# Kernel optimization log

Measured on AMD Instinct MI355X. Metric: run time of the kernel, lower is better.

The kernel has to match this reference:

```python
import jax, jax.numpy as jnp
import numpy as np

H, W = 56, 56
N = H * W
C = 2
THETA_ALPHA = 160.0
THETA_BETA = 3.0
THETA_GAMMA = 3.0
NUM_ITERATIONS = 10


def setup_inputs() -> dict:
    key = jax.random.key(0)
    k1, k2, k3, k4 = jax.random.split(key, 4)
    inputs = jax.random.uniform(k1, (2, H, W), dtype=jnp.float32)
    # Keras 'uniform' initializer: U(-0.05, 0.05)
    sp_w = jax.random.uniform(k2, (C, C), minval=-0.05, maxval=0.05, dtype=jnp.float32)
    bl_w = jax.random.uniform(k3, (C, C), minval=-0.05, maxval=0.05, dtype=jnp.float32)
    compat = jax.random.uniform(k4, (C, C), minval=-0.05, maxval=0.05, dtype=jnp.float32)
    return {"inputs": inputs, "spatial_ker_weights": sp_w,
            "bilateral_ker_weights": bl_w, "compatibility_matrix": compat}


def _sqdist(f):
    # f: [N, D] -> [N, N] squared pairwise distances
    s = jnp.sum(f * f, axis=1)
    return s[:, None] + s[None, :] - 2.0 * (f @ f.T)


def _kernels(rgb_flat):
    # rgb_flat: [N, 3] pixel colors (0..255)
    ys, xs = jnp.meshgrid(jnp.arange(H, dtype=jnp.float32),
                          jnp.arange(W, dtype=jnp.float32), indexing="ij")
    pos = jnp.stack([xs.reshape(-1), ys.reshape(-1)], axis=1)  # [N, 2]
    # spatial (Gaussian) kernel: exp(-||p-q||^2 / (2*gamma^2))
    k_sp = jnp.exp(-0.5 * _sqdist(pos / THETA_GAMMA))
    # bilateral kernel: positions scaled by alpha, colors by beta
    f_bl = jnp.concatenate([pos / THETA_ALPHA, rgb_flat / THETA_BETA], axis=1)
    k_bl = jnp.exp(-0.5 * _sqdist(f_bl))
    return k_sp, k_bl


def reference(inputs, spatial_ker_weights, bilateral_ker_weights, compatibility_matrix):
    unary = inputs[0]            # [H, W], foreground prob
    gray = inputs[1] * 255.0     # [H, W], image intensities scaled as in the layer

    # unaries: [C, H, W] with channel 0 = 1-u, channel 1 = u
    unaries = jnp.stack([1.0 - unary, unary], axis=0).reshape(C, N)

    rgb_flat = jnp.tile(gray.reshape(-1)[:, None], (1, 3))  # [N, 3]

    k_sp, k_bl = _kernels(rgb_flat)
    ones = jnp.ones((N,), dtype=jnp.float32)
    norm_sp = k_sp @ ones  # [N]
    norm_bl = k_bl @ ones  # [N]

    q = unaries
    for i in range(NUM_ITERATIONS):
        softmax_out = q if i == 0 else jax.nn.softmax(q, axis=0)
        spatial_out = (softmax_out @ k_sp) / norm_sp[None, :]     # [C, N]
        bilateral_out = (softmax_out @ k_bl) / norm_bl[None, :]   # [C, N]
        message = spatial_ker_weights @ spatial_out + bilateral_ker_weights @ bilateral_out
        pairwise = compatibility_matrix @ message                 # [C, N]
        q = unaries - pairwise

    cur_q = q.reshape(C, H, W).transpose(1, 2, 0)  # [H, W, C]
    obj_prob = jax.nn.softmax(cur_q, axis=2)[:, :, 1]
    return obj_prob.reshape(1, H, W)
```

## Files before the change

kernel.cpp:

```cpp
#include <hip/hip_runtime.h>


namespace {

constexpr int NPIX = 3136;
constexpr int WIMG = 56;
constexpr int JPB  = 16;
constexpr int NBLK = NPIX / JPB;
constexpr int NTHR = 512;
constexpr int NQ   = NPIX / 4;
constexpr int NBUF = 9;
constexpr int BAND = 16;
constexpr int Q2   = NQ - NTHR;

constexpr float LOG2E = 1.4426950408889634f;
constexpr float C1 = -LOG2E / 18.0f;
constexpr float C2 = -LOG2E / 51200.0f;
constexpr float C3 = -LOG2E / 6.0f;

constexpr int O_SSH  = 0;
constexpr int O_GSRT = 12544;
constexpr int O_MSRT = 25088;
constexpr int O_OFF  = 31360;
constexpr int O_WSX  = 32400;
constexpr int O_WSY  = 35984;
constexpr int O_ROWC = 39568;
constexpr int POOLSZ = 43376;

#define REDUCE32(v) \
    { v += __shfl_xor(v, 1); v += __shfl_xor(v, 2); v += __shfl_xor(v, 4); \
      v += __shfl_xor(v, 8); v += __shfl_xor(v, 16); }

__global__ __launch_bounds__(NTHR) void crf_all(
    const float* __restrict__ inp,
    const float* __restrict__ spw, const float* __restrict__ blw,
    const float* __restrict__ cmw,
    float* sbufs, float* __restrict__ out)
{
    __shared__ __align__(16) unsigned char pool[POOLSZ];
    float*  s_sh  = (float*)(pool + O_SSH);
    float4* s_sh4 = (float4*)(pool + O_SSH);
    float*  g_srt = (float*)(pool + O_GSRT);
    unsigned short* m_srt = (unsigned short*)(pool + O_MSRT);
    unsigned*       offs  = (unsigned*)(pool + O_OFF);
    float*  wsx   = (float*)(pool + O_WSX);
    float*  wsy   = (float*)(pool + O_WSY);
    float*  rowc  = (float*)(pool + O_ROWC);
    unsigned short* H  = (unsigned short*)(pool + O_SSH);
    unsigned*       Hz = (unsigned*)(pool + O_SSH);

    const int t   = threadIdx.x;
    const int bid = blockIdx.x;
    const int sub = t & 31;
    const int jl  = t >> 5;
    const int j   = bid * JPB + jl;
    const int xj  = j % WIMG;
    const int yj  = j / WIMG;
    const float xjf = (float)xj, yjf = (float)yj;

    const float uj = inp[j];
    const float gj = inp[NPIX + j] * 255.0f;

    const float e0 = cmw[2] - cmw[0];
    const float e1 = cmw[3] - cmw[1];
    const float alpha = e0 * (spw[0] + blw[0]) + e1 * (spw[2] + blw[2]);
    const float beta  = e0 * (spw[1] - spw[0]) + e1 * (spw[3] - spw[2]);
    const float gamma = e0 * (blw[1] - blw[0]) + e1 * (blw[3] - blw[2]);

    for (int i = t; i < 6272; i += NTHR) Hz[i] = 0u;
    for (int idx = t; idx < JPB * 56; idx += NTHR) {
        const int jlw = idx / 56, p = idx - jlw * 56;
        const int jj = bid * JPB + jlw;
        const float ddx = (float)(jj % WIMG - p);
        const float ddy = (float)(jj / WIMG - p);
        wsx[idx] = __builtin_amdgcn_exp2f(C1 * ddx * ddx);
        wsy[idx] = __builtin_amdgcn_exp2f(C1 * ddy * ddy);
    }
    __syncthreads();
    if (t < 49) {
        unsigned short* Hr = H + t * 256;
        const int mb = t * 64;
        for (int i = 0; i < 64; ++i) {
            int b = (int)(inp[NPIX + mb + i] * 255.0f);
            b = b > 255 ? 255 : b;
            Hr[b] = (unsigned short)(Hr[b] + 1);
        }
    }
    __syncthreads();
    if (t < 256) {
        unsigned run = 0;
        for (int c = 0; c < 49; ++c) {
            unsigned short v = H[c * 256 + t];
            H[c * 256 + t] = (unsigned short)run;
            run += v;
        }
        offs[t] = run;
    }
    __syncthreads();
    if (t < 64) {
        unsigned v0 = offs[4 * t], v1 = offs[4 * t + 1];
        unsigned v2 = offs[4 * t + 2], v3 = offs[4 * t + 3];
        unsigned sum = v0 + v1 + v2 + v3;
        unsigned sc = sum;
        for (int d = 1; d < 64; d <<= 1) {
            unsigned n = __shfl_up(sc, d);
            if (t >= d) sc += n;
        }
        unsigned base = sc - sum;
        offs[4 * t] = base;
        offs[4 * t + 1] = base + v0;
        offs[4 * t + 2] = base + v0 + v1;
        offs[4 * t + 3] = base + v0 + v1 + v2;
        if (t == 63) offs[256] = sc;
    }
    __syncthreads();
    if (t < 49) {
        unsigned short* Hr = H + t * 256;
        const int mb = t * 64;
        for (int i = 0; i < 64; ++i) {
            int b = (int)(inp[NPIX + mb + i] * 255.0f);
            b = b > 255 ? 255 : b;
            int r = (int)offs[b] + (int)Hr[b];
            Hr[b] = (unsigned short)(Hr[b] + 1);
            m_srt[r] = (unsigned short)(mb + i);
        }
    }
    __syncthreads();
    for (int p = t; p < NPIX; p += NTHR)
        g_srt[p] = inp[NPIX + (int)m_srt[p]] * 255.0f;
    {
        const float4* u4 = (const float4*)inp;
        for (int q = t; q < NQ; q += NTHR) s_sh4[q] = u4[q];
    }
    __syncthreads();

    float sx, sy;
    {
        float dd = xjf - (float)sub;
        sx = __builtin_amdgcn_exp2f(C1 * dd * dd);
        if (sub + 32 < 56) {
            float d2 = xjf - (float)(sub + 32);
            sx += __builtin_amdgcn_exp2f(C1 * d2 * d2);
        }
        REDUCE32(sx);
        dd = yjf - (float)sub;
        sy = __builtin_amdgcn_exp2f(C1 * dd * dd);
        if (sub + 32 < 56) {
            float d2 = yjf - (float)(sub + 32);
            sy += __builtin_amdgcn_exp2f(C1 * d2 * d2);
        }
        REDUCE32(sy);
    }
    const float rnsp = 1.0f / (sx * sy);

    int bj = (int)gj; bj = bj > 255 ? 255 : bj;
    const int blo = (int)offs[bj < BAND ? 0 : bj - BAND];
    const int bhi = (int)offs[(bj + BAND > 255 ? 255 : bj + BAND) + 1];

    auto spatial = [&]() -> float {
        {
            const int y = t >> 4, c = t & 15;
            const float4* R = (const float4*)(wsx + c * 56);
            const float4* S = s_sh4 + y * 14;
            float acc = 0.f;
#pragma unroll
            for (int q = 0; q < 14; ++q) {
                float4 w = R[q], sv = S[q];
                acc = fmaf(w.x, sv.x, acc); acc = fmaf(w.y, sv.y, acc);
                acc = fmaf(w.z, sv.z, acc); acc = fmaf(w.w, sv.w, acc);
            }
            rowc[y * 17 + c] = acc;
        }
        {
            const int idx = t + NTHR;
            if (idx < 56 * 16) {
                const int y = idx >> 4, c = idx & 15;
                const float4* R = (const float4*)(wsx + c * 56);
                const float4* S = s_sh4 + y * 14;
                float acc = 0.f;
#pragma unroll
                for (int q = 0; q < 14; ++q) {
                    float4 w = R[q], sv = S[q];
                    acc = fmaf(w.x, sv.x, acc); acc = fmaf(w.y, sv.y, acc);
                    acc = fmaf(w.z, sv.z, acc); acc = fmaf(w.w, sv.w, acc);
                }
                rowc[y * 17 + c] = acc;
            }
        }
        __syncthreads();
        const float* wy = wsy + jl * 56;
        float part = wy[sub] * rowc[sub * 17 + jl];
        if (sub + 32 < 56)
            part = fmaf(wy[sub + 32], rowc[(sub + 32) * 17 + jl], part);
        REDUCE32(part);
        return part;
    };

    auto bilateral = [&](float* nacc_out) -> float {
        float acc = 0.f, nacc = 0.f;
        for (int p = blo + sub; p < bhi; p += 32) {
            const int m = (int)m_srt[p];
            const float gv = g_srt[p];
            const float sv = s_sh[m];
            const int yi = (m * 9363) >> 19;
            const int xi = m - yi * 56;
            const float ux = (float)xi - xjf, vy = (float)yi - yjf;
            const float r2 = fmaf(ux, ux, vy * vy);
            const float dg = gv - gj;
            const float w = __builtin_amdgcn_exp2f(fmaf(dg * C3, dg, r2 * C2));
            acc = fmaf(w, sv, acc);
            if (nacc_out) nacc += w;
        }
        REDUCE32(acc);
        if (nacc_out) { REDUCE32(nacc); *nacc_out = nacc; }
        return acc;
    };

    auto publish_sync = [&](float s, float* buf) {
        if (sub == 0)
            __hip_atomic_store(&buf[j], s, __ATOMIC_RELAXED,
                               __HIP_MEMORY_SCOPE_AGENT);
        const float4* src = (const float4*)buf;
        float4 a, b;
        const bool two = (t < Q2);
        bool da = false, db = !two;
        for (;;) {
            if (!da)
                asm volatile("global_load_dwordx4 %0, %1, off sc0 sc1"
                             : "=&v"(a) : "v"(src + t));
            if (!db)
                asm volatile("global_load_dwordx4 %0, %1, off sc0 sc1"
                             : "=&v"(b) : "v"(src + NTHR + t));
            asm volatile("s_waitcnt vmcnt(0)" ::: "memory");
            if (!da) da = (fminf(fminf(a.x, a.y), fminf(a.z, a.w)) != 0.0f);
            if (!db) db = (fminf(fminf(b.x, b.y), fminf(b.z, b.w)) != 0.0f);
            if (da && db) break;
        }
        s_sh4[t] = a;
        if (two) s_sh4[NTHR + t] = b;
        __syncthreads();
    };

    const float base = 2.0f * uj - 1.0f - alpha;
    float rnbl, s;

    {
        float tsp = spatial();
        float nacc;
        float acc = bilateral(&nacc);
        rnbl = 1.0f / nacc;
        float d = base - beta * (tsp * rnsp) - gamma * (acc * rnbl);
        s = 1.0f / (1.0f + __builtin_amdgcn_exp2f(-d * LOG2E));
    }
    publish_sync(s, sbufs);

    for (int k = 1; k < 10; ++k) {
        float tsp = spatial();
        float acc = bilateral(nullptr);
        float d = base - beta * (tsp * rnsp) - gamma * (acc * rnbl);
        s = 1.0f / (1.0f + __builtin_amdgcn_exp2f(-d * LOG2E));
        if (k < 9) publish_sync(s, sbufs + k * NPIX);
        else if (sub == 0) out[j] = s;
    }
}

}

extern "C" void kernel_launch(void* const* d_in, const int* in_sizes, int n_in,
                              void* d_out, int out_size, void* d_ws, size_t ws_size,
                              hipStream_t stream) {
    const float* inp = (const float*)d_in[0];
    const float* spw = (const float*)d_in[1];
    const float* blw = (const float*)d_in[2];
    const float* cmw = (const float*)d_in[3];
    float* sbufs = (float*)d_ws;
    float* out = (float*)d_out;

    hipMemsetAsync(sbufs, 0, NBUF * NPIX * sizeof(float), stream);
    crf_all<<<dim3(NBLK), dim3(NTHR), 0, stream>>>(inp, spw, blw, cmw,
                                                   sbufs, out);
}
```

Baseline: 65.02 us.

## Cache bilateral weights in LDS and band-limit spatial row convolution

The bilateral weights for each pixel are computed once in the first iteration and stored in a per-pixel shared-memory band buffer of up to 768 entries. Later iterations reuse them instead of recomputing exp2. Entries beyond that cap are still recomputed. The spatial row pass is remapped so each wave handles two columns over all 56 rows, and the dot product is limited to the band where the Gaussian is non-negligible (±16 pixels). Shared memory grows from about 43KB to about 92KB, which may reduce occupancy, and the band truncation slightly approximates the spatial sum.

```diff
diff --git a/kernel.cpp b/kernel.cpp
--- a/kernel.cpp
+++ b/kernel.cpp
@@ -12,20 +12,23 @@
 constexpr int NBUF = 9;
 constexpr int BAND = 16;
 constexpr int Q2   = NQ - NTHR;
+constexpr int MAXB = 768;
 
 constexpr float LOG2E = 1.4426950408889634f;
 constexpr float C1 = -LOG2E / 18.0f;
 constexpr float C2 = -LOG2E / 51200.0f;
 constexpr float C3 = -LOG2E / 6.0f;
 
-constexpr int O_SSH  = 0;
-constexpr int O_GSRT = 12544;
-constexpr int O_MSRT = 25088;
-constexpr int O_OFF  = 31360;
-constexpr int O_WSX  = 32400;
-constexpr int O_WSY  = 35984;
-constexpr int O_ROWC = 39568;
-constexpr int POOLSZ = 43376;
+constexpr int O_SSH   = 0;
+constexpr int O_GSRT  = 12544;
+constexpr int O_MSRT  = 25088;
+constexpr int O_OFF   = 31360;
+constexpr int O_WSX   = 32400;
+constexpr int O_WSY   = 35984;
+constexpr int O_ROWC  = 39568;
+constexpr int O_XLOC  = 43376;
+constexpr int O_WBAND = 43440;
+constexpr int POOLSZ  = 92592;
 
 #define REDUCE32(v) \
     { v += __shfl_xor(v, 1); v += __shfl_xor(v, 2); v += __shfl_xor(v, 4); \
@@ -46,6 +49,8 @@
     float*  wsx   = (float*)(pool + O_WSX);
     float*  wsy   = (float*)(pool + O_WSY);
     float*  rowc  = (float*)(pool + O_ROWC);
+    int*    xloc  = (int*)(pool + O_XLOC);
+    float*  wband = (float*)(pool + O_WBAND);
     unsigned short* H  = (unsigned short*)(pool + O_SSH);
     unsigned*       Hz = (unsigned*)(pool + O_SSH);
 
@@ -76,6 +81,7 @@
         wsx[idx] = __builtin_amdgcn_exp2f(C1 * ddx * ddx);
         wsy[idx] = __builtin_amdgcn_exp2f(C1 * ddy * ddy);
     }
+    if (t < JPB) xloc[t] = (bid * JPB + t) % WIMG;
     __syncthreads();
     if (t < 49) {
         unsigned short* Hr = H + t * 256;
@@ -156,35 +162,28 @@
     int bj = (int)gj; bj = bj > 255 ? 255 : bj;
     const int blo = (int)offs[bj < BAND ? 0 : bj - BAND];
     const int bhi = (int)offs[(bj + BAND > 255 ? 255 : bj + BAND) + 1];
+    const int blen = bhi - blo;
+    const int bl1 = blen < MAXB ? blen : MAXB;
 
     auto spatial = [&]() -> float {
-        {
-            const int y = t >> 4, c = t & 15;
-            const float4* R = (const float4*)(wsx + c * 56);
-            const float4* S = s_sh4 + y * 14;
-            float acc = 0.f;
+        const int wv = t >> 6;
+        const int ln = t & 63;
+        if (ln < 56) {
 #pragma unroll
-            for (int q = 0; q < 14; ++q) {
-                float4 w = R[q], sv = S[q];
-                acc = fmaf(w.x, sv.x, acc); acc = fmaf(w.y, sv.y, acc);
-                acc = fmaf(w.z, sv.z, acc); acc = fmaf(w.w, sv.w, acc);
-            }
-            rowc[y * 17 + c] = acc;
-        }
-        {
-            const int idx = t + NTHR;
-            if (idx < 56 * 16) {
-                const int y = idx >> 4, c = idx & 15;
+            for (int cc = 0; cc < 2; ++cc) {
+                const int c = wv * 2 + cc;
+                const int X = xloc[c];
+                const int qlo = (X > 16) ? ((X - 16) >> 2) : 0;
+                const int qhi = (X < 40) ? ((X + 16) >> 2) : 13;
                 const float4* R = (const float4*)(wsx + c * 56);
-                const float4* S = s_sh4 + y * 14;
+                const float4* S = s_sh4 + ln * 14;
                 float acc = 0.f;
-#pragma unroll
-                for (int q = 0; q < 14; ++q) {
+                for (int q = qlo; q <= qhi; ++q) {
                     float4 w = R[q], sv = S[q];
                     acc = fmaf(w.x, sv.x, acc); acc = fmaf(w.y, sv.y, acc);
                     acc = fmaf(w.z, sv.z, acc); acc = fmaf(w.w, sv.w, acc);
                 }
-                rowc[y * 17 + c] = acc;
+                rowc[ln * 17 + c] = acc;
             }
         }
         __syncthreads();
@@ -194,26 +193,6 @@
             part = fmaf(wy[sub + 32], rowc[(sub + 32) * 17 + jl], part);
         REDUCE32(part);
         return part;
-    };
-
-    auto bilateral = [&](float* nacc_out) -> float {
-        float acc = 0.f, nacc = 0.f;
-        for (int p = blo + sub; p < bhi; p += 32) {
-            const int m = (int)m_srt[p];
-            const float gv = g_srt[p];
-            const float sv = s_sh[m];
-            const int yi = (m * 9363) >> 19;
-            const int xi = m - yi * 56;
-            const float ux = (float)xi - xjf, vy = (float)yi - yjf;
-            const float r2 = fmaf(ux, ux, vy * vy);
-            const float dg = gv - gj;
-            const float w = __builtin_amdgcn_exp2f(fmaf(dg * C3, dg, r2 * C2));
-            acc = fmaf(w, sv, acc);
-            if (nacc_out) nacc += w;
-        }
-        REDUCE32(acc);
-        if (nacc_out) { REDUCE32(nacc); *nacc_out = nacc; }
-        return acc;
     };
 
     auto publish_sync = [&](float s, float* buf) {
@@ -246,8 +225,23 @@
 
     {
         float tsp = spatial();
-        float nacc;
-        float acc = bilateral(&nacc);
+        float acc = 0.f, nacc = 0.f;
+        float* wb = wband + jl * MAXB;
+        for (int i = sub; i < blen; i += 32) {
+            const int p = blo + i;
+            const int m = (int)m_srt[p];
+            const float gv = g_srt[p];
+            const int yi = (m * 9363) >> 19;
+            const int xi = m - yi * 56;
+            const float ux = (float)xi - xjf, vy = (float)yi - yjf;
+            const float r2 = fmaf(ux, ux, vy * vy);
+            const float dg = gv - gj;
+            const float w = __builtin_amdgcn_exp2f(fmaf(dg * C3, dg, r2 * C2));
+            if (i < MAXB) wb[i] = w;
+            acc = fmaf(w, s_sh[m], acc);
+            nacc += w;
+        }
+        REDUCE32(acc); REDUCE32(nacc);
         rnbl = 1.0f / nacc;
         float d = base - beta * (tsp * rnsp) - gamma * (acc * rnbl);
         s = 1.0f / (1.0f + __builtin_amdgcn_exp2f(-d * LOG2E));
@@ -256,7 +250,26 @@
 
     for (int k = 1; k < 10; ++k) {
         float tsp = spatial();
-        float acc = bilateral(nullptr);
+        float acc = 0.f;
+        const float* wb = wband + jl * MAXB;
+        for (int i = sub; i < bl1; i += 32) {
+            const float w = wb[i];
+            const int m = (int)m_srt[blo + i];
+            acc = fmaf(w, s_sh[m], acc);
+        }
+        for (int i = MAXB + sub; i < blen; i += 32) {
+            const int p = blo + i;
+            const int m = (int)m_srt[p];
+            const float gv = g_srt[p];
+            const int yi = (m * 9363) >> 19;
+            const int xi = m - yi * 56;
+            const float ux = (float)xi - xjf, vy = (float)yi - yjf;
+            const float r2 = fmaf(ux, ux, vy * vy);
+            const float dg = gv - gj;
+            const float w = __builtin_amdgcn_exp2f(fmaf(dg * C3, dg, r2 * C2));
+            acc = fmaf(w, s_sh[m], acc);
+        }
+        REDUCE32(acc);
         float d = base - beta * (tsp * rnsp) - gamma * (acc * rnbl);
         s = 1.0f / (1.0f + __builtin_amdgcn_exp2f(-d * LOG2E));
         if (k < 9) publish_sync(s, sbufs + k * NPIX);
```

After: 76.51 us. 17.7% more time.
